# Performance work log

Hardware: AMD Instinct MI355X
Metric: run time of the kernel (lower is better)

Reference implementation:

```python
import jax, jax.numpy as jnp
import numpy as np

B, H, N, F, P, NODE = 64, 168, 512, 8, 24, 0


def _lstm(x, k, rk, b, return_sequences):
    # x: (B, T, Fin); keras LSTM gate order i, f, g(c), o
    Bx = x.shape[0]
    U = rk.shape[0]
    h0 = jnp.zeros((Bx, U), x.dtype)

    def step(carry, xt):
        h, c = carry
        z = xt @ k + h @ rk + b
        i, f, g, o = jnp.split(z, 4, axis=-1)
        c = jax.nn.sigmoid(f) * c + jax.nn.sigmoid(i) * jnp.tanh(g)
        h = jax.nn.sigmoid(o) * jnp.tanh(c)
        return (h, c), h

    (_, _), hs = jax.lax.scan(step, (h0, h0), jnp.swapaxes(x, 0, 1))
    return jnp.swapaxes(hs, 0, 1) if return_sequences else hs[-1]


def _node_summaries(inputs):
    # inputs: (B, H, N, F). Per-(b,n) temporal stats over H of feature 0.
    x0 = inputs[..., 0]                      # (B, H, N)
    mean_full = x0.mean(axis=1)              # (B, N)
    mean_half = x0[:, H // 2:].mean(axis=1)
    std_full = x0.std(axis=1)                # population std (ddof=0), like tf
    std_half = x0[:, H // 2:].std(axis=1)
    c = x0 - mean_full[:, None, :]
    m2 = (c * c).mean(axis=1)
    m3 = (c ** 3).mean(axis=1)
    m4 = (c ** 4).mean(axis=1)
    skew = jnp.nan_to_num(m3 / m2 ** 1.5)    # scipy.stats.skew (biased)
    kurt = jnp.nan_to_num(m4 / (m2 * m2) - 3.0)  # scipy Fisher kurtosis
    t = jnp.arange(H, dtype=x0.dtype)
    tc = t - t.mean()
    slope = jnp.nan_to_num(jnp.einsum('h,bhn->bn', tc, x0) / (tc * tc).sum())
    return jnp.stack([mean_full, mean_half, std_full, std_half, skew, kurt, slope], axis=2)  # (B, N, 7)


def reference(inputs, adj, w_gcn1, b_gcn1, w_gcn2, b_gcn2, w_conv1, b_conv1,
              w_conv2, b_conv2, k_lstm1, rk_lstm1, b_lstm1, k_lstm2, rk_lstm2,
              b_lstm2, w_out, b_out):
    nf = _node_summaries(inputs)                                   # (B, N, 7)
    # GraphConv: relu(A @ X @ W + b)
    h = jax.nn.relu(jnp.einsum('nm,bmc->bnc', adj, nf @ w_gcn1) + b_gcn1)
    g = jax.nn.relu(jnp.einsum('nm,bmc->bnc', adj, h @ w_gcn2) + b_gcn2)   # (B, N, 16)
    # Conv1D channels_first: channels = N, steps = 16
    dn = ('NCH', 'HIO', 'NCH')
    c1 = jax.lax.conv_general_dilated(g, w_conv1, (1,), 'SAME', dimension_numbers=dn) + b_conv1[None, :, None]  # (B,4,16)
    p = c1.reshape(B, 4, 8, 2).mean(axis=-1)                        # AveragePooling1D(2)  (B,4,8)
    c2 = jax.lax.conv_general_dilated(p, w_conv2, (1,), 'SAME', dimension_numbers=dn) + b_conv2[None, :, None]  # (B,4,8)
    gcn_out = jnp.concatenate([c2.reshape(B, -1), p.reshape(B, -1)], axis=-1)  # skip connection, (B, 64)
    # LSTM stack on the selected node's time series
    seq = inputs[:, :, NODE, :]                                     # (B, H, F)
    l1 = _lstm(seq, k_lstm1, rk_lstm1, b_lstm1, True)
    l2 = _lstm(l1, k_lstm2, rk_lstm2, b_lstm2, False)               # (B, 128)
    out = jnp.concatenate([gcn_out, l2], axis=-1)                   # (B, 192); dropout is identity at inference
    return out @ w_out + b_out                                      # (B, P)


def setup_inputs() -> dict:
    key = jax.random.key(0)
    ks = jax.random.split(key, 16)
    s = 0.05
    return {
        'inputs': jax.random.normal(ks[0], (B, H, N, F), jnp.float32),
        'adj': jax.random.uniform(ks[1], (N, N), jnp.float32) / N,
        'w_gcn1': jax.random.normal(ks[2], (7, 32), jnp.float32) * s,
        'b_gcn1': jnp.zeros((32,), jnp.float32),
        'w_gcn2': jax.random.normal(ks[3], (32, 16), jnp.float32) * s,
        'b_gcn2': jnp.zeros((16,), jnp.float32),
        'w_conv1': jax.random.normal(ks[4], (3, N, 4), jnp.float32) * s,
        'b_conv1': jnp.zeros((4,), jnp.float32),
        'w_conv2': jax.random.normal(ks[5], (3, 4, 4), jnp.float32) * s,
        'b_conv2': jnp.zeros((4,), jnp.float32),
        'k_lstm1': jax.random.normal(ks[6], (F, 512), jnp.float32) * s,
        'rk_lstm1': jax.random.normal(ks[7], (128, 512), jnp.float32) * s,
        'b_lstm1': jnp.zeros((512,), jnp.float32),
        'k_lstm2': jax.random.normal(ks[8], (128, 512), jnp.float32) * s,
        'rk_lstm2': jax.random.normal(ks[9], (128, 512), jnp.float32) * s,
        'b_lstm2': jnp.zeros((512,), jnp.float32),
        'w_out': jax.random.normal(ks[10], (192, P), jnp.float32) * s,
        'b_out': jnp.zeros((P,), jnp.float32),
    }
```

## Files before the change

kernel.cpp:

```cpp
#include <hip/hip_runtime.h>
#include <cstdint>
#include <cstddef>

#define BB 64
#define HH 168
#define NN 512
#define FF 8
#define UL 128
#define GD 512

__device__ __forceinline__ float sigf(float x){ return 1.0f/(1.0f+__expf(-x)); }
__device__ __forceinline__ float tanhfast(float x){ return 1.0f - 2.0f/(1.0f+__expf(2.0f*x)); }

__global__ __launch_bounds__(256) void k_sum(const float* __restrict__ in, float* __restrict__ ps){
  int bid = blockIdx.x;
  int b = bid>>2, nh = (bid>>1)&1, hh = bid&1;
  int n = nh*256 + threadIdx.x;
  int h0 = hh*84;
  const float* p = in + ((size_t)(b*HH + h0)*NN + n)*FF;
  float s1=0.f,s2=0.f,s3=0.f,s4=0.f,st=0.f;
  #pragma unroll 4
  for(int h=0;h<84;++h){
    float x = p[(size_t)h*NN*FF];
    float hc = (float)(h+h0) - 83.5f;
    s1 += x;
    float x2 = x*x;
    s2 += x2;
    s3 += x2*x;
    s4 += x2*x2;
    st += hc*x;
  }
  float* o = ps + ((size_t)((b*NN+n)*2 + hh))*8;
  o[0]=s1; o[1]=s2; o[2]=s3; o[3]=s4; o[4]=st;
}

__global__ __launch_bounds__(256) void k_sumc(const float* __restrict__ ps, float* __restrict__ nf){
  int idx = blockIdx.x*256 + threadIdx.x;
  const float* a = ps + (size_t)idx*16;
  const float* c2 = a + 8;
  float s1 = a[0]+c2[0], s2 = a[1]+c2[1], s3 = a[2]+c2[2], s4 = a[3]+c2[3], st = a[4]+c2[4];
  float s1h = c2[0], s2h = c2[1];
  const float iH = 1.0f/168.0f, iHh = 1.0f/84.0f;
  float mean = s1*iH, meanh = s1h*iHh;
  float ex2 = s2*iH, ex3 = s3*iH, ex4 = s4*iH;
  float m2 = ex2 - mean*mean;
  float m3 = ex3 - 3.0f*mean*ex2 + 2.0f*mean*mean*mean;
  float m4 = ex4 - 4.0f*mean*ex3 + 6.0f*mean*mean*ex2 - 3.0f*mean*mean*mean*mean;
  m2 = fmaxf(m2, 0.0f);
  float stdf = sqrtf(m2);
  float m2h = fmaxf(s2h*iHh - meanh*meanh, 0.0f);
  float stdh = sqrtf(m2h);
  float denom = m2*stdf;
  float skew = denom > 0.0f ? m3/denom : 0.0f;
  float kurt = m2 > 0.0f ? (m4/(m2*m2) - 3.0f) : 0.0f;
  float slope = st * (1.0f/395122.0f);
  float* o = nf + (size_t)idx*7;
  o[0]=mean; o[1]=meanh; o[2]=stdf; o[3]=stdh; o[4]=skew; o[5]=kurt; o[6]=slope;
}

__global__ __launch_bounds__(256) void k_gcn1(const float* __restrict__ nf, const float* __restrict__ adj,
        const float* __restrict__ w1, const float* __restrict__ b1, float* __restrict__ h1){
  __shared__ float t_s[NN*32];
  __shared__ float adj_s[128*68];
  int b = blockIdx.x>>2, n0 = (blockIdx.x&3)*128;
  int tid = threadIdx.x;
  {
    int c = tid&31;
    float w1c[7];
    #pragma unroll
    for(int k=0;k<7;++k) w1c[k] = w1[k*32+c];
    for(int idx=tid; idx<NN*32; idx+=256){
      int m = idx>>5;
      const float* nfp = nf + (size_t)(b*NN+m)*7;
      float acc = 0.f;
      #pragma unroll
      for(int k=0;k<7;++k) acc += nfp[k]*w1c[k];
      t_s[idx] = acc;
    }
  }
  int c2 = tid&15, nl = tid>>4;
  float acc[8][2];
  #pragma unroll
  for(int j=0;j<8;++j){acc[j][0]=0.f;acc[j][1]=0.f;}
  for(int mt=0; mt<8; ++mt){
    __syncthreads();
    for(int idx=tid; idx<128*64; idx+=256){
      int r = idx>>6, cc = idx&63;
      adj_s[r*68+cc] = adj[(size_t)(n0+r)*NN + mt*64 + cc];
    }
    __syncthreads();
    for(int mm=0; mm<64; mm+=4){
      float2 tv[4];
      #pragma unroll
      for(int q=0;q<4;++q) tv[q] = *(const float2*)&t_s[(mt*64+mm+q)*32 + 2*c2];
      #pragma unroll
      for(int j=0;j<8;++j){
        float4 a4 = *(const float4*)&adj_s[(nl+16*j)*68 + mm];
        acc[j][0] += a4.x*tv[0].x + a4.y*tv[1].x + a4.z*tv[2].x + a4.w*tv[3].x;
        acc[j][1] += a4.x*tv[0].y + a4.y*tv[1].y + a4.z*tv[2].y + a4.w*tv[3].y;
      }
    }
  }
  float bb0 = b1[2*c2], bb1 = b1[2*c2+1];
  #pragma unroll
  for(int j=0;j<8;++j){
    int n = n0 + nl + 16*j;
    float2 v;
    v.x = fmaxf(acc[j][0]+bb0, 0.0f);
    v.y = fmaxf(acc[j][1]+bb1, 0.0f);
    *(float2*)&h1[(size_t)(b*NN+n)*32 + 2*c2] = v;
  }
}

__global__ __launch_bounds__(256) void k_gcn2(const float* __restrict__ h1, const float* __restrict__ adj,
        const float* __restrict__ w2, const float* __restrict__ b2, float* __restrict__ g){
  __shared__ float t_s[NN*16];
  __shared__ float adj_s[128*68];
  int b = blockIdx.x>>2, n0 = (blockIdx.x&3)*128;
  int tid = threadIdx.x;
  {
    int jh = tid&7;
    float w2c0[32], w2c1[32];
    #pragma unroll
    for(int c=0;c<32;++c){ w2c0[c] = w2[c*16+2*jh]; w2c1[c] = w2[c*16+2*jh+1]; }
    for(int idx=tid; idx<NN*8; idx+=256){
      int m = idx>>3;
      const float4* hp = (const float4*)(h1 + (size_t)(b*NN+m)*32);
      float a0=0.f, a1=0.f;
      #pragma unroll
      for(int q=0;q<8;++q){
        float4 hv = hp[q];
        a0 += hv.x*w2c0[4*q] + hv.y*w2c0[4*q+1] + hv.z*w2c0[4*q+2] + hv.w*w2c0[4*q+3];
        a1 += hv.x*w2c1[4*q] + hv.y*w2c1[4*q+1] + hv.z*w2c1[4*q+2] + hv.w*w2c1[4*q+3];
      }
      t_s[m*16+2*jh] = a0;
      t_s[m*16+2*jh+1] = a1;
    }
  }
  int j = tid&15, nl = tid>>4;
  float acc[8];
  #pragma unroll
  for(int q=0;q<8;++q) acc[q]=0.f;
  for(int mt=0; mt<8; ++mt){
    __syncthreads();
    for(int idx=tid; idx<128*64; idx+=256){
      int r = idx>>6, cc = idx&63;
      adj_s[r*68+cc] = adj[(size_t)(n0+r)*NN + mt*64 + cc];
    }
    __syncthreads();
    for(int mm=0; mm<64; mm+=4){
      float tv[4];
      #pragma unroll
      for(int q=0;q<4;++q) tv[q] = t_s[(mt*64+mm+q)*16 + j];
      #pragma unroll
      for(int q=0;q<8;++q){
        float4 a4 = *(const float4*)&adj_s[(nl+16*q)*68 + mm];
        acc[q] += a4.x*tv[0] + a4.y*tv[1] + a4.z*tv[2] + a4.w*tv[3];
      }
    }
  }
  float bbj = b2[j];
  #pragma unroll
  for(int q=0;q<8;++q){
    int n = n0 + nl + 16*q;
    g[(size_t)(b*NN+n)*16 + j] = fmaxf(acc[q]+bbj, 0.0f);
  }
}

__global__ __launch_bounds__(256) void k_conv(const float* __restrict__ g, const float* __restrict__ wc1,
        const float* __restrict__ bc1, const float* __restrict__ wc2, const float* __restrict__ bc2,
        float* __restrict__ feat){
  __shared__ float g_s[NN*16];
  __shared__ float w1_s[3*NN*4];
  __shared__ float c1p[4][4][16];
  __shared__ float c1_s[4][16];
  __shared__ float p_s[4][8];
  int b = blockIdx.x, tid = threadIdx.x;
  for(int idx=tid; idx<NN*16; idx+=256) g_s[idx] = g[(size_t)b*NN*16 + idx];
  for(int idx=tid; idx<3*NN*4; idx+=256) w1_s[idx] = wc1[idx];
  __syncthreads();
  {
    int q = tid>>6, p = tid&63, o = p>>4, x = p&15;
    int c0 = q*128;
    float acc = 0.f;
    #pragma unroll
    for(int k=0;k<3;++k){
      int xx = x + k - 1;
      if(xx>=0 && xx<16){
        #pragma unroll 4
        for(int c=c0;c<c0+128;++c) acc += g_s[c*16+xx]*w1_s[(k*NN+c)*4+o];
      }
    }
    c1p[q][o][x] = acc;
  }
  __syncthreads();
  if(tid<64){
    int o = tid>>4, x = tid&15;
    c1_s[o][x] = c1p[0][o][x]+c1p[1][o][x]+c1p[2][o][x]+c1p[3][o][x] + bc1[o];
  }
  __syncthreads();
  if(tid<32){
    int oo = tid>>3, xp = tid&7;
    float pv = 0.5f*(c1_s[oo][2*xp]+c1_s[oo][2*xp+1]);
    p_s[oo][xp] = pv;
    feat[b*192 + 32 + oo*8 + xp] = pv;
  }
  __syncthreads();
  if(tid<32){
    int oo = tid>>3, x2 = tid&7;
    float a2 = bc2[oo];
    #pragma unroll
    for(int k=0;k<3;++k){
      int xx = x2 + k - 1;
      if(xx>=0 && xx<8){
        #pragma unroll
        for(int c=0;c<4;++c) a2 += p_s[c][xx]*wc2[(k*4+c)*4+oo];
      }
    }
    feat[b*192 + oo*8 + x2] = a2;
  }
}

__global__ __launch_bounds__(512,2) void k_lstm1(const float* __restrict__ in, const float* __restrict__ k1,
        const float* __restrict__ rk1, const float* __restrict__ b1, float* __restrict__ l1){
  __shared__ float seq_s[HH*FF];
  __shared__ float h_s2[4*36];
  __shared__ float a_s[GD];
  int b = blockIdx.x, tid = threadIdx.x;
  int q = tid&3, grp = tid>>2;
  bool q0 = (tid&1)!=0, q1 = (tid&2)!=0;
  float4 w4[32];
  {
    const float4* rkp = (const float4*)rk1;
    #pragma unroll
    for(int k=0;k<32;++k) w4[k] = rkp[(size_t)(q*32+k)*(GD/4) + grp];
  }
  float wkx[FF];
  #pragma unroll
  for(int f=0;f<FF;++f) wkx[f] = k1[f*GD+tid];
  float bz = b1[tid];
  for(int idx=tid; idx<HH*FF; idx+=512)
    seq_s[idx] = in[(size_t)(b*HH + (idx>>3))*NN*FF + (idx&7)];
  if(tid<UL) h_s2[(tid>>5)*36 + (tid&31)] = 0.0f;
  float c = 0.0f;
  __syncthreads();
  const float4* hq = (const float4*)&h_s2[q*36];
  #pragma unroll 1
  for(int t=0;t<HH;++t){
    float4 x0 = *(const float4*)&seq_s[t*FF];
    float4 x1 = *(const float4*)&seq_s[t*FF+4];
    float zx = bz + x0.x*wkx[0]+x0.y*wkx[1]+x0.z*wkx[2]+x0.w*wkx[3]
                  + x1.x*wkx[4]+x1.y*wkx[5]+x1.z*wkx[6]+x1.w*wkx[7];
    float p0=0.f,p1=0.f,p2=0.f,p3=0.f;
    #pragma unroll
    for(int j=0;j<8;++j){
      float4 hv = hq[j];
      p0 += hv.x*w4[4*j].x + hv.y*w4[4*j+1].x + hv.z*w4[4*j+2].x + hv.w*w4[4*j+3].x;
      p1 += hv.x*w4[4*j].y + hv.y*w4[4*j+1].y + hv.z*w4[4*j+2].y + hv.w*w4[4*j+3].y;
      p2 += hv.x*w4[4*j].z + hv.y*w4[4*j+1].z + hv.z*w4[4*j+2].z + hv.w*w4[4*j+3].z;
      p3 += hv.x*w4[4*j].w + hv.y*w4[4*j+1].w + hv.z*w4[4*j+2].w + hv.w*w4[4*j+3].w;
    }
    float send0 = q0 ? p0 : p1;
    float send1 = q0 ? p2 : p3;
    float r0 = __shfl_xor(send0, 1);
    float r1 = __shfl_xor(send1, 1);
    float s0 = (q0 ? p1 : p0) + r0;
    float s1 = (q0 ? p3 : p2) + r1;
    float send2 = q1 ? s0 : s1;
    float r2 = __shfl_xor(send2, 2);
    float z = zx + (q1 ? s1 : s0) + r2;
    float act = ((tid>>7)==2) ? tanhfast(z) : sigf(z);
    a_s[tid] = act;
    __syncthreads();
    int u = tid&127;
    float ia=a_s[u], fa=a_s[UL+u], ga=a_s[2*UL+u], oa=a_s[3*UL+u];
    c = fa*c + ia*ga;
    float hn = oa*tanhfast(c);
    if(tid<UL){
      h_s2[(tid>>5)*36 + (tid&31)] = hn;
      l1[((size_t)b*HH + t)*UL + tid] = hn;
    }
    __syncthreads();
  }
}

__global__ __launch_bounds__(256) void k_zin2(const float* __restrict__ l1, const float* __restrict__ k2,
        const float* __restrict__ b2, float* __restrict__ zin){
  __shared__ float l_s[21*UL];
  int b = blockIdx.x>>3, t0 = (blockIdx.x&7)*21;
  int tid = threadIdx.x;
  for(int idx=tid; idx<21*UL; idx+=256)
    l_s[idx] = l1[((size_t)b*HH + t0 + (idx>>7))*UL + (idx&127)];
  __syncthreads();
  float acc0[21], acc1[21];
  #pragma unroll
  for(int q=0;q<21;++q){acc0[q]=0.f;acc1[q]=0.f;}
  for(int j=0;j<UL;j+=4){
    float kv00=k2[j*GD+tid],     kv01=k2[(j+1)*GD+tid],     kv02=k2[(j+2)*GD+tid],     kv03=k2[(j+3)*GD+tid];
    float kv10=k2[j*GD+tid+256], kv11=k2[(j+1)*GD+tid+256], kv12=k2[(j+2)*GD+tid+256], kv13=k2[(j+3)*GD+tid+256];
    #pragma unroll
    for(int q=0;q<21;++q){
      float4 lv = *(const float4*)&l_s[q*UL + j];
      acc0[q] += lv.x*kv00 + lv.y*kv01 + lv.z*kv02 + lv.w*kv03;
      acc1[q] += lv.x*kv10 + lv.y*kv11 + lv.z*kv12 + lv.w*kv13;
    }
  }
  float bb0 = b2[tid], bb1 = b2[tid+256];
  #pragma unroll
  for(int q=0;q<21;++q){
    zin[((size_t)b*HH + t0 + q)*GD + tid]       = acc0[q] + bb0;
    zin[((size_t)b*HH + t0 + q)*GD + tid + 256] = acc1[q] + bb1;
  }
}

__global__ __launch_bounds__(512,2) void k_lstm2(const float* __restrict__ zin, const float* __restrict__ rk2,
        float* __restrict__ feat){
  __shared__ float h_s2[4*36];
  __shared__ float a_s[GD];
  int b = blockIdx.x, tid = threadIdx.x;
  int q = tid&3, grp = tid>>2;
  bool q0 = (tid&1)!=0, q1 = (tid&2)!=0;
  float4 w4[32];
  {
    const float4* rkp = (const float4*)rk2;
    #pragma unroll
    for(int k=0;k<32;++k) w4[k] = rkp[(size_t)(q*32+k)*(GD/4) + grp];
  }
  if(tid<UL) h_s2[(tid>>5)*36 + (tid&31)] = 0.0f;
  float c = 0.0f;
  float zc = zin[((size_t)b*HH)*GD + tid];
  __syncthreads();
  const float4* hq = (const float4*)&h_s2[q*36];
  #pragma unroll 1
  for(int t=0;t<HH;++t){
    float nz = 0.f;
    if(t+1<HH) nz = zin[((size_t)b*HH+t+1)*GD + tid];
    float p0=0.f,p1=0.f,p2=0.f,p3=0.f;
    #pragma unroll
    for(int j=0;j<8;++j){
      float4 hv = hq[j];
      p0 += hv.x*w4[4*j].x + hv.y*w4[4*j+1].x + hv.z*w4[4*j+2].x + hv.w*w4[4*j+3].x;
      p1 += hv.x*w4[4*j].y + hv.y*w4[4*j+1].y + hv.z*w4[4*j+2].y + hv.w*w4[4*j+3].y;
      p2 += hv.x*w4[4*j].z + hv.y*w4[4*j+1].z + hv.z*w4[4*j+2].z + hv.w*w4[4*j+3].z;
      p3 += hv.x*w4[4*j].w + hv.y*w4[4*j+1].w + hv.z*w4[4*j+2].w + hv.w*w4[4*j+3].w;
    }
    float send0 = q0 ? p0 : p1;
    float send1 = q0 ? p2 : p3;
    float r0 = __shfl_xor(send0, 1);
    float r1 = __shfl_xor(send1, 1);
    float s0 = (q0 ? p1 : p0) + r0;
    float s1 = (q0 ? p3 : p2) + r1;
    float send2 = q1 ? s0 : s1;
    float r2 = __shfl_xor(send2, 2);
    float z = zc + (q1 ? s1 : s0) + r2;
    float act = ((tid>>7)==2) ? tanhfast(z) : sigf(z);
    a_s[tid] = act;
    __syncthreads();
    int u = tid&127;
    float ia=a_s[u], fa=a_s[UL+u], ga=a_s[2*UL+u], oa=a_s[3*UL+u];
    c = fa*c + ia*ga;
    float hn = oa*tanhfast(c);
    if(tid<UL){
      h_s2[(tid>>5)*36 + (tid&31)] = hn;
      if(t==HH-1) feat[b*192 + 64 + tid] = hn;
    }
    __syncthreads();
    zc = nz;
  }
}

__global__ __launch_bounds__(256) void k_out(const float* __restrict__ feat, const float* __restrict__ wo,
        const float* __restrict__ bo, float* __restrict__ out){
  int idx = blockIdx.x*256 + threadIdx.x;
  if(idx >= BB*24) return;
  int b = idx/24, p = idx - b*24;
  float a0 = bo[p], a1 = 0.f, a2 = 0.f, a3 = 0.f;
  const float* f = feat + b*192;
  for(int k=0;k<192;k+=4){
    a0 += f[k]*wo[k*24+p];
    a1 += f[k+1]*wo[(k+1)*24+p];
    a2 += f[k+2]*wo[(k+2)*24+p];
    a3 += f[k+3]*wo[(k+3)*24+p];
  }
  out[idx] = (a0+a1)+(a2+a3);
}

extern "C" void kernel_launch(void* const* d_in, const int* in_sizes, int n_in,
                              void* d_out, int out_size, void* d_ws, size_t ws_size,
                              hipStream_t stream){
  const float* inp = (const float*)d_in[0];
  const float* adj = (const float*)d_in[1];
  const float* w1  = (const float*)d_in[2];
  const float* b1  = (const float*)d_in[3];
  const float* w2  = (const float*)d_in[4];
  const float* b2  = (const float*)d_in[5];
  const float* wc1 = (const float*)d_in[6];
  const float* bc1 = (const float*)d_in[7];
  const float* wc2 = (const float*)d_in[8];
  const float* bc2 = (const float*)d_in[9];
  const float* k1  = (const float*)d_in[10];
  const float* rk1 = (const float*)d_in[11];
  const float* bl1 = (const float*)d_in[12];
  const float* k2  = (const float*)d_in[13];
  const float* rk2 = (const float*)d_in[14];
  const float* bl2 = (const float*)d_in[15];
  const float* wo  = (const float*)d_in[16];
  const float* bo  = (const float*)d_in[17];
  float* out = (float*)d_out;
  float* ws = (float*)d_ws;

  float* ps   = ws;
  float* nf   = ps + 524288;
  float* h1   = nf + 229376;
  float* g    = h1 + 1048576;
  float* feat = g  + 524288;
  float* l1   = feat + 12288;
  float* zin  = l1 + 1376256;

  k_sum  <<<dim3(256), dim3(256), 0, stream>>>(inp, ps);
  k_sumc <<<dim3(128), dim3(256), 0, stream>>>(ps, nf);
  k_gcn1 <<<dim3(256), dim3(256), 0, stream>>>(nf, adj, w1, b1, h1);
  k_gcn2 <<<dim3(256), dim3(256), 0, stream>>>(h1, adj, w2, b2, g);
  k_conv <<<dim3(64),  dim3(256), 0, stream>>>(g, wc1, bc1, wc2, bc2, feat);
  k_lstm1<<<dim3(64),  dim3(512), 0, stream>>>(inp, k1, rk1, bl1, l1);
  k_zin2 <<<dim3(512), dim3(256), 0, stream>>>(l1, k2, bl2, zin);
  k_lstm2<<<dim3(64),  dim3(512), 0, stream>>>(zin, rk2, feat);
  k_out  <<<dim3(6),   dim3(256), 0, stream>>>(feat, wo, bo, out);
}
```

Measured before the change: 433.5 us.

## Split LSTM recurrent weights between LDS and global; branchless rcp activations

Both LSTM kernels stop holding all 128 recurrent-weight floats per thread in registers. They stage 12 of the 32 float4 rows into a 96KB LDS buffer in a remapped layout and re-read the other 20 rows from global memory on every time step. The gate activation becomes one branchless form built on the hardware reciprocal, selected by per-thread constants. This frees VGPRs, but it puts extra LDS reads and cached global loads on the serial per-step critical path. The large LDS footprint also limits how many blocks fit per CU.

Measured after the change: 468.2 us. 8.0% more time.

```diff
diff --git a/kernel.cpp b/kernel.cpp
--- a/kernel.cpp
+++ b/kernel.cpp
@@ -9,8 +9,7 @@
 #define UL 128
 #define GD 512
 
-__device__ __forceinline__ float sigf(float x){ return 1.0f/(1.0f+__expf(-x)); }
-__device__ __forceinline__ float tanhfast(float x){ return 1.0f - 2.0f/(1.0f+__expf(2.0f*x)); }
+__device__ __forceinline__ float frcp(float x){ return __builtin_amdgcn_rcpf(x); }
 
 __global__ __launch_bounds__(256) void k_sum(const float* __restrict__ in, float* __restrict__ ps){
   int bid = blockIdx.x;
@@ -223,28 +222,35 @@
 
 __global__ __launch_bounds__(512,2) void k_lstm1(const float* __restrict__ in, const float* __restrict__ k1,
         const float* __restrict__ rk1, const float* __restrict__ b1, float* __restrict__ l1){
+  __shared__ float4 wlds[6144];
   __shared__ float seq_s[HH*FF];
   __shared__ float h_s2[4*36];
   __shared__ float a_s[GD];
   int b = blockIdx.x, tid = threadIdx.x;
   int q = tid&3, grp = tid>>2;
+  int w_ = tid>>6, l = tid&63;
   bool q0 = (tid&1)!=0, q1 = (tid&2)!=0;
-  float4 w4[32];
-  {
-    const float4* rkp = (const float4*)rk1;
-    #pragma unroll
-    for(int k=0;k<32;++k) w4[k] = rkp[(size_t)(q*32+k)*(GD/4) + grp];
+  const float4* rkp = (const float4*)rk1;
+  for(int g = tid; g < 6144; g += 512){
+    int r = g>>7;
+    int qq = r/12, k = r - qq*12;
+    int col4 = g&127;
+    int w2 = col4>>4, jj = col4&15;
+    wlds[(w2*12+k)*64 + jj*4 + qq] = rkp[(size_t)(qq*32+k)*(GD/4) + col4];
   }
   float wkx[FF];
   #pragma unroll
   for(int f=0;f<FF;++f) wkx[f] = k1[f*GD+tid];
   float bz = b1[tid];
+  bool isg = ((tid>>7)==2);
+  float Ac = isg?1.f:0.f, Bc = isg?-2.f:1.f, Sc = isg?2.f:-1.f;
   for(int idx=tid; idx<HH*FF; idx+=512)
     seq_s[idx] = in[(size_t)(b*HH + (idx>>3))*NN*FF + (idx&7)];
   if(tid<UL) h_s2[(tid>>5)*36 + (tid&31)] = 0.0f;
   float c = 0.0f;
   __syncthreads();
   const float4* hq = (const float4*)&h_s2[q*36];
+  const float4* wl = &wlds[(w_*12)*64 + l];
   #pragma unroll 1
   for(int t=0;t<HH;++t){
     float4 x0 = *(const float4*)&seq_s[t*FF];
@@ -253,29 +259,46 @@
                   + x1.x*wkx[4]+x1.y*wkx[5]+x1.z*wkx[6]+x1.w*wkx[7];
     float p0=0.f,p1=0.f,p2=0.f,p3=0.f;
     #pragma unroll
-    for(int j=0;j<8;++j){
-      float4 hv = hq[j];
-      p0 += hv.x*w4[4*j].x + hv.y*w4[4*j+1].x + hv.z*w4[4*j+2].x + hv.w*w4[4*j+3].x;
-      p1 += hv.x*w4[4*j].y + hv.y*w4[4*j+1].y + hv.z*w4[4*j+2].y + hv.w*w4[4*j+3].y;
-      p2 += hv.x*w4[4*j].z + hv.y*w4[4*j+1].z + hv.z*w4[4*j+2].z + hv.w*w4[4*j+3].z;
-      p3 += hv.x*w4[4*j].w + hv.y*w4[4*j+1].w + hv.z*w4[4*j+2].w + hv.w*w4[4*j+3].w;
+    for(int kk=0;kk<3;++kk){
+      float4 hv = hq[kk];
+      float4 wa = wl[(4*kk+0)*64];
+      float4 wb = wl[(4*kk+1)*64];
+      float4 wc = wl[(4*kk+2)*64];
+      float4 wd = wl[(4*kk+3)*64];
+      p0 += hv.x*wa.x + hv.y*wb.x + hv.z*wc.x + hv.w*wd.x;
+      p1 += hv.x*wa.y + hv.y*wb.y + hv.z*wc.y + hv.w*wd.y;
+      p2 += hv.x*wa.z + hv.y*wb.z + hv.z*wc.z + hv.w*wd.z;
+      p3 += hv.x*wa.w + hv.y*wb.w + hv.z*wc.w + hv.w*wd.w;
+    }
+    #pragma unroll
+    for(int kk=0;kk<5;++kk){
+      float4 hv = hq[3+kk];
+      float4 wa = rkp[(size_t)(q*32+12+4*kk+0)*(GD/4) + grp];
+      float4 wb = rkp[(size_t)(q*32+12+4*kk+1)*(GD/4) + grp];
+      float4 wc = rkp[(size_t)(q*32+12+4*kk+2)*(GD/4) + grp];
+      float4 wd = rkp[(size_t)(q*32+12+4*kk+3)*(GD/4) + grp];
+      p0 += hv.x*wa.x + hv.y*wb.x + hv.z*wc.x + hv.w*wd.x;
+      p1 += hv.x*wa.y + hv.y*wb.y + hv.z*wc.y + hv.w*wd.y;
+      p2 += hv.x*wa.z + hv.y*wb.z + hv.z*wc.z + hv.w*wd.z;
+      p3 += hv.x*wa.w + hv.y*wb.w + hv.z*wc.w + hv.w*wd.w;
     }
     float send0 = q0 ? p0 : p1;
     float send1 = q0 ? p2 : p3;
     float r0 = __shfl_xor(send0, 1);
     float r1 = __shfl_xor(send1, 1);
     float s0 = (q0 ? p1 : p0) + r0;
-    float s1 = (q0 ? p3 : p2) + r1;
-    float send2 = q1 ? s0 : s1;
+    float s1v = (q0 ? p3 : p2) + r1;
+    float send2 = q1 ? s0 : s1v;
     float r2 = __shfl_xor(send2, 2);
-    float z = zx + (q1 ? s1 : s0) + r2;
-    float act = ((tid>>7)==2) ? tanhfast(z) : sigf(z);
+    float z = zx + (q1 ? s1v : s0) + r2;
+    float act = Ac + Bc*frcp(1.0f + __expf(Sc*z));
     a_s[tid] = act;
     __syncthreads();
     int u = tid&127;
     float ia=a_s[u], fa=a_s[UL+u], ga=a_s[2*UL+u], oa=a_s[3*UL+u];
     c = fa*c + ia*ga;
-    float hn = oa*tanhfast(c);
+    float th = 1.0f - 2.0f*frcp(1.0f + __expf(2.0f*c));
+    float hn = oa*th;
     if(tid<UL){
       h_s2[(tid>>5)*36 + (tid&31)] = hn;
       l1[((size_t)b*HH + t)*UL + tid] = hn;
@@ -315,51 +338,75 @@
 
 __global__ __launch_bounds__(512,2) void k_lstm2(const float* __restrict__ zin, const float* __restrict__ rk2,
         float* __restrict__ feat){
+  __shared__ float4 wlds[6144];
   __shared__ float h_s2[4*36];
   __shared__ float a_s[GD];
   int b = blockIdx.x, tid = threadIdx.x;
   int q = tid&3, grp = tid>>2;
+  int w_ = tid>>6, l = tid&63;
   bool q0 = (tid&1)!=0, q1 = (tid&2)!=0;
-  float4 w4[32];
-  {
-    const float4* rkp = (const float4*)rk2;
-    #pragma unroll
-    for(int k=0;k<32;++k) w4[k] = rkp[(size_t)(q*32+k)*(GD/4) + grp];
-  }
+  const float4* rkp = (const float4*)rk2;
+  for(int g = tid; g < 6144; g += 512){
+    int r = g>>7;
+    int qq = r/12, k = r - qq*12;
+    int col4 = g&127;
+    int w2 = col4>>4, jj = col4&15;
+    wlds[(w2*12+k)*64 + jj*4 + qq] = rkp[(size_t)(qq*32+k)*(GD/4) + col4];
+  }
+  bool isg = ((tid>>7)==2);
+  float Ac = isg?1.f:0.f, Bc = isg?-2.f:1.f, Sc = isg?2.f:-1.f;
   if(tid<UL) h_s2[(tid>>5)*36 + (tid&31)] = 0.0f;
   float c = 0.0f;
-  float zc = zin[((size_t)b*HH)*GD + tid];
+  float zc = zin[(size_t)b*HH*GD + tid];
   __syncthreads();
   const float4* hq = (const float4*)&h_s2[q*36];
+  const float4* wl = &wlds[(w_*12)*64 + l];
   #pragma unroll 1
   for(int t=0;t<HH;++t){
     float nz = 0.f;
-    if(t+1<HH) nz = zin[((size_t)b*HH+t+1)*GD + tid];
+    if(t+1<HH) nz = zin[((size_t)b*HH + t+1)*GD + tid];
     float p0=0.f,p1=0.f,p2=0.f,p3=0.f;
     #pragma unroll
-    for(int j=0;j<8;++j){
-      float4 hv = hq[j];
-      p0 += hv.x*w4[4*j].x + hv.y*w4[4*j+1].x + hv.z*w4[4*j+2].x + hv.w*w4[4*j+3].x;
-      p1 += hv.x*w4[4*j].y + hv.y*w4[4*j+1].y + hv.z*w4[4*j+2].y + hv.w*w4[4*j+3].y;
-      p2 += hv.x*w4[4*j].z + hv.y*w4[4*j+1].z + hv.z*w4[4*j+2].z + hv.w*w4[4*j+3].z;
-      p3 += hv.x*w4[4*j].w + hv.y*w4[4*j+1].w + hv.z*w4[4*j+2].w + hv.w*w4[4*j+3].w;
+    for(int kk=0;kk<3;++kk){
+      float4 hv = hq[kk];
+      float4 wa = wl[(4*kk+0)*64];
+      float4 wb = wl[(4*kk+1)*64];
+      float4 wc = wl[(4*kk+2)*64];
+      float4 wd = wl[(4*kk+3)*64];
+      p0 += hv.x*wa.x + hv.y*wb.x + hv.z*wc.x + hv.w*wd.x;
+      p1 += hv.x*wa.y + hv.y*wb.y + hv.z*wc.y + hv.w*wd.y;
+      p2 += hv.x*wa.z + hv.y*wb.z + hv.z*wc.z + hv.w*wd.z;
+      p3 += hv.x*wa.w + hv.y*wb.w + hv.z*wc.w + hv.w*wd.w;
+    }
+    #pragma unroll
+    for(int kk=0;kk<5;++kk){
+      float4 hv = hq[3+kk];
+      float4 wa = rkp[(size_t)(q*32+12+4*kk+0)*(GD/4) + grp];
+      float4 wb = rkp[(size_t)(q*32+12+4*kk+1)*(GD/4) + grp];
+      float4 wc = rkp[(size_t)(q*32+12+4*kk+2)*(GD/4) + grp];
+      float4 wd = rkp[(size_t)(q*32+12+4*kk+3)*(GD/4) + grp];
+      p0 += hv.x*wa.x + hv.y*wb.x + hv.z*wc.x + hv.w*wd.x;
+      p1 += hv.x*wa.y + hv.y*wb.y + hv.z*wc.y + hv.w*wd.y;
+      p2 += hv.x*wa.z + hv.y*wb.z + hv.z*wc.z + hv.w*wd.z;
+      p3 += hv.x*wa.w + hv.y*wb.w + hv.z*wc.w + hv.w*wd.w;
     }
     float send0 = q0 ? p0 : p1;
     float send1 = q0 ? p2 : p3;
     float r0 = __shfl_xor(send0, 1);
     float r1 = __shfl_xor(send1, 1);
     float s0 = (q0 ? p1 : p0) + r0;
-    float s1 = (q0 ? p3 : p2) + r1;
-    float send2 = q1 ? s0 : s1;
+    float s1v = (q0 ? p3 : p2) + r1;
+    float send2 = q1 ? s0 : s1v;
     float r2 = __shfl_xor(send2, 2);
-    float z = zc + (q1 ? s1 : s0) + r2;
-    float act = ((tid>>7)==2) ? tanhfast(z) : sigf(z);
+    float z = zc + (q1 ? s1v : s0) + r2;
+    float act = Ac + Bc*frcp(1.0f + __expf(Sc*z));
     a_s[tid] = act;
     __syncthreads();
     int u = tid&127;
     float ia=a_s[u], fa=a_s[UL+u], ga=a_s[2*UL+u], oa=a_s[3*UL+u];
     c = fa*c + ia*ga;
-    float hn = oa*tanhfast(c);
+    float th = 1.0f - 2.0f*frcp(1.0f + __expf(2.0f*c));
+    float hn = oa*th;
     if(tid<UL){
       h_s2[(tid>>5)*36 + (tid&31)] = hn;
       if(t==HH-1) feat[b*192 + 64 + tid] = hn;
```
